# Performance work log

Hardware: AMD Instinct MI355X
Metric: run time of the kernel (lower is better)

The kernel has to match this reference:

```python
import jax, jax.numpy as jnp
import numpy as np

C1, C2, NUM_HEADS = 128, 128, 8
N, H_A, W_A = 2, 200, 200
H_B, W_B = 100, 360


def _polar_coords(fov, gh, gw, H, W):
    # Pixel-space polar sampling grid, matching torch linspace semantics.
    cx, cy = W // 2, H // 2
    t = jnp.arange(gw, dtype=jnp.float32) / (gw - 1)
    angles = -fov / 2 + fov * t                      # [gw]
    ca, sa = jnp.cos(angles), jnp.sin(angles)
    rmax = jnp.minimum(cx / jnp.abs(ca), cy / jnp.abs(sa))
    r = (jnp.arange(gh, dtype=jnp.float32) / (gh - 1))[:, None] * rmax[None, :]  # [gh,gw]
    x = jnp.clip(cx + r * ca, 0.0, W - 1.0)
    y = jnp.clip(cy - r * sa, 0.0, H - 1.0)
    return x, y


def _bilinear(bev, x, y):
    # grid_sample(mode='bilinear', align_corners=True) with in-range clamped coords.
    C, H, W = bev.shape
    x0 = jnp.floor(x); y0 = jnp.floor(y)
    wx = x - x0; wy = y - y0
    x0i = jnp.clip(x0.astype(jnp.int32), 0, W - 1)
    x1i = jnp.clip(x0i + 1, 0, W - 1)
    y0i = jnp.clip(y0.astype(jnp.int32), 0, H - 1)
    y1i = jnp.clip(y0i + 1, 0, H - 1)
    v00 = bev[:, y0i, x0i]; v01 = bev[:, y0i, x1i]
    v10 = bev[:, y1i, x0i]; v11 = bev[:, y1i, x1i]
    return v00 * (1 - wx) * (1 - wy) + v01 * wx * (1 - wy) + v10 * (1 - wx) * wy + v11 * wx * wy


def _restore(rect, fov, H, W):
    # scatter-add restore with count normalization (rrestore_bev_map).
    C, gh, gw = rect.shape
    x, y = _polar_coords(fov, gh, gw, H, W)
    xi = jnp.clip(jnp.round(x).astype(jnp.int32), 0, W - 1)
    yi = jnp.clip(jnp.round(y).astype(jnp.int32), 0, H - 1)
    idx = (yi * W + xi).reshape(-1)
    vals = rect.reshape(C, -1)
    acc = jnp.zeros((C, H * W), rect.dtype).at[:, idx].add(vals)
    cnt = jnp.zeros((H * W,), rect.dtype).at[idx].add(jnp.ones_like(idx, rect.dtype))
    cnt = jnp.where(cnt == 0, jnp.ones_like(cnt), cnt)
    return (acc / cnt).reshape(C, H, W)


def _mha(q, k, v, in_w, in_b, out_w, out_b, nheads):
    # torch.nn.MultiheadAttention (batch_first, eval mode -> dropout inactive).
    B, Lq, E = q.shape
    Lk = k.shape[1]
    hd = E // nheads
    wq, wk, wv = jnp.split(in_w, 3)
    bq, bk, bv = jnp.split(in_b, 3)
    qh = (q @ wq.T + bq).reshape(B, Lq, nheads, hd).transpose(0, 2, 1, 3)
    kh = (k @ wk.T + bk).reshape(B, Lk, nheads, hd).transpose(0, 2, 1, 3)
    vh = (v @ wv.T + bv).reshape(B, Lk, nheads, hd).transpose(0, 2, 1, 3)
    scores = jnp.einsum('bhqd,bhkd->bhqk', qh, kh) / jnp.sqrt(jnp.asarray(hd, q.dtype))
    attn = jax.nn.softmax(scores, axis=-1)
    o = jnp.einsum('bhqk,bhkd->bhqd', attn, vh).transpose(0, 2, 1, 3).reshape(B, Lq, E)
    return o @ out_w.T + out_b


def setup_inputs() -> dict:
    key = jax.random.key(0)
    ks = jax.random.split(key, 12)
    s1 = 1.0 / np.sqrt(C1)
    s2 = 1.0 / np.sqrt(C2)
    return {
        'list_a': jax.random.normal(ks[0], (N, C1, H_A, W_A), jnp.float32),
        'list_b': jax.random.normal(ks[1], (N, C2, H_B, W_B), jnp.float32),
        'fov_list': jax.random.uniform(ks[2], (N,), jnp.float32, 0.5 * np.pi, 0.9 * np.pi),
        'rots_list': jax.random.normal(ks[3], (N, 3, 3), jnp.float32),
        'trans_list': jax.random.normal(ks[4], (N, 3), jnp.float32),
        'Wq': jax.random.normal(ks[5], (C1, C1), jnp.float32) * s1,
        'bq': jnp.zeros((C1,), jnp.float32),
        'Wk': jax.random.normal(ks[6], (C1, C2), jnp.float32) * s2,
        'bk': jnp.zeros((C1,), jnp.float32),
        'Wv': jax.random.normal(ks[7], (C1, C2), jnp.float32) * s2,
        'bv': jnp.zeros((C1,), jnp.float32),
        'in_proj_w': jax.random.normal(ks[8], (3 * C1, C1), jnp.float32) * s1,
        'in_proj_b': jnp.zeros((3 * C1,), jnp.float32),
        'out_w': jax.random.normal(ks[9], (C1, C1), jnp.float32) * s1,
        'out_b': jnp.zeros((C1,), jnp.float32),
    }


def reference(list_a, list_b, fov_list, rots_list, trans_list,
              Wq, bq, Wk, bk, Wv, bv, in_proj_w, in_proj_b, out_w, out_b):
    def per_sample(a, b, fov):
        c1, h1, w1 = a.shape
        c2, h2, w2 = b.shape
        # extract rectangular (polar resample) of a onto (h1, w2) grid
        x, y = _polar_coords(fov, h1, w2, h1, w1)
        a_rect = _bilinear(a, x, y)                 # [C1, h1, w2]
        a_seq = a_rect.transpose(2, 1, 0)           # [w2, h1, C1]
        b_seq = b.transpose(2, 1, 0)                # [w2, h2, C2]
        q = a_seq @ Wq.T + bq
        k = b_seq @ Wk.T + bk
        v = b_seq @ Wv.T + bv
        o = _mha(q, k, v, in_proj_w, in_proj_b, out_w, out_b, NUM_HEADS)
        a_enh = o.transpose(2, 1, 0)                # [C1, h1, w2]
        return a + _restore(a_enh, fov, h1, w1)
    return jax.vmap(per_sample)(list_a, list_b, fov_list)
```

## Files before the change

### kernel.cpp

```cpp
#include <hip/hip_runtime.h>
#include <hip/hip_bf16.h>
#include <math.h>

#define C1N 128
#define HA 200
#define WA 200
#define HBB 100
#define WBB 360
#define GH 200
#define GW 360
#define NHD 8
#define HDD 16

typedef __attribute__((ext_vector_type(8))) short short8;
typedef __attribute__((ext_vector_type(4))) float f32x4;
typedef __attribute__((ext_vector_type(16))) float f32x16;

__device__ __forceinline__ float bf2f(unsigned short u) {
  union { unsigned int i; float f; } c; c.i = ((unsigned int)u) << 16; return c.f;
}
__device__ __forceinline__ unsigned short f2bf(float f) {
  __hip_bfloat16 h = __float2bfloat16(f);
  unsigned short u;
  __builtin_memcpy(&u, &h, sizeof(u));
  return u;
}

__device__ __forceinline__ void polar_xy(float fov, int i, int j, float& x, float& y) {
#pragma clang fp contract(off)
  float t = (float)j / 359.0f;
  float angle = -fov / 2.0f + fov * t;
  float ca = (float)cos((double)angle);
  float sa = (float)sin((double)angle);
  float rmax = fminf(100.0f / fabsf(ca), 100.0f / fabsf(sa));
  float r = ((float)i / 199.0f) * rmax;
  float xv = 100.0f + r * ca;
  float yv = 100.0f - r * sa;
  x = fminf(fmaxf(xv, 0.0f), 199.0f);
  y = fminf(fmaxf(yv, 0.0f), 199.0f);
}

__global__ void weff_k(const float* __restrict__ Wq, const float* __restrict__ Wk,
                       const float* __restrict__ Wv, const float* __restrict__ bq,
                       const float* __restrict__ bk, const float* __restrict__ bv,
                       const float* __restrict__ inw, const float* __restrict__ inb,
                       const float* __restrict__ outw, const float* __restrict__ outb,
                       __hip_bfloat16* __restrict__ Wb, float* __restrict__ beff) {
  int which = blockIdx.y;
  int o = blockIdx.x;
  int kcol = threadIdx.x;
  if (which == 3) {
    Wb[3 * 16384 + o * 128 + kcol] = __float2bfloat16(outw[o * 128 + kcol]);
    if (kcol == 0) beff[384 + o] = outb[o];
    return;
  }
  const float* Wx = (which == 0) ? Wq : ((which == 1) ? Wk : Wv);
  const float* bx = (which == 0) ? bq : ((which == 1) ? bk : bv);
  const float* wrow = inw + (which * 128 + o) * 128;
  float acc = 0.0f;
  for (int m = 0; m < 128; ++m) acc += wrow[m] * Wx[m * 128 + kcol];
  Wb[which * 16384 + o * 128 + kcol] = __float2bfloat16(acc);
  if (kcol == 0) {
    float bacc = inb[which * 128 + o];
    for (int m = 0; m < 128; ++m) bacc += wrow[m] * bx[m];
    beff[which * 128 + o] = bacc;
  }
}

__global__ __launch_bounds__(256) void transA_k(const float* __restrict__ a,
                                                __hip_bfloat16* __restrict__ aT) {
  __shared__ float tile[32][33];
  int p0 = blockIdx.x * 32, c0 = blockIdx.y * 32;
  int tp = threadIdx.x & 31, tr = threadIdx.x >> 5;
  for (int cc = tr; cc < 32; cc += 8)
    tile[cc][tp] = a[(size_t)(c0 + cc) * 40000 + p0 + tp];
  __syncthreads();
  for (int pp = tr; pp < 32; pp += 8)
    aT[(size_t)(p0 + pp) * C1N + c0 + tp] = __float2bfloat16(tile[tp][pp]);
}

__global__ __launch_bounds__(256) void bilinear2_k(const __hip_bfloat16* __restrict__ aT,
                                                   const float* __restrict__ fovp, int n,
                                                   __hip_bfloat16* __restrict__ aseq) {
  __shared__ float sw[20][4];
  __shared__ int sp[20][4];
  int j = blockIdx.x;
  int i_base = blockIdx.y * 20;
  int t = threadIdx.x;
  if (t < 20) {
    float x, y;
    polar_xy(fovp[n], i_base + t, j, x, y);
    float x0f = floorf(x), y0f = floorf(y);
    float wx = x - x0f, wy = y - y0f;
    int x0 = max(0, min(199, (int)x0f));
    int x1 = min(x0 + 1, 199);
    int y0 = max(0, min(199, (int)y0f));
    int y1 = min(y0 + 1, 199);
    sp[t][0] = y0 * 200 + x0; sp[t][1] = y0 * 200 + x1;
    sp[t][2] = y1 * 200 + x0; sp[t][3] = y1 * 200 + x1;
    sw[t][0] = (1.0f - wx) * (1.0f - wy); sw[t][1] = wx * (1.0f - wy);
    sw[t][2] = (1.0f - wx) * wy;          sw[t][3] = wx * wy;
  }
  __syncthreads();
  int lane = t & 63, wv = t >> 6;
  for (int ii = wv; ii < 20; ii += 4) {
    int i = i_base + ii;
    float w00 = sw[ii][0], w01 = sw[ii][1], w10 = sw[ii][2], w11 = sw[ii][3];
    ushort2 u00 = ((const ushort2*)(aT + (size_t)sp[ii][0] * C1N))[lane];
    ushort2 u01 = ((const ushort2*)(aT + (size_t)sp[ii][1] * C1N))[lane];
    ushort2 u10 = ((const ushort2*)(aT + (size_t)sp[ii][2] * C1N))[lane];
    ushort2 u11 = ((const ushort2*)(aT + (size_t)sp[ii][3] * C1N))[lane];
    float v0 = w00 * bf2f(u00.x) + w01 * bf2f(u01.x) + w10 * bf2f(u10.x) + w11 * bf2f(u11.x);
    float v1 = w00 * bf2f(u00.y) + w01 * bf2f(u01.y) + w10 * bf2f(u10.y) + w11 * bf2f(u11.y);
    ushort2 outv; outv.x = f2bf(v0); outv.y = f2bf(v1);
    ((ushort2*)(aseq + (size_t)(j * GH + i) * C1N))[lane] = outv;
  }
}

__global__ __launch_bounds__(256) void transpose_k(const float* __restrict__ b,
                                                   __hip_bfloat16* __restrict__ bs) {
  __shared__ float tile[32][33];
  int kk = blockIdx.z;
  int j0 = blockIdx.x * 32, c0 = blockIdx.y * 32;
  int tj = threadIdx.x & 31;
  int tr = threadIdx.x >> 5;
  for (int cc = tr; cc < 32; cc += 8) {
    int gj = j0 + tj;
    tile[cc][tj] = (gj < WBB) ? b[(c0 + cc) * (HBB * WBB) + kk * WBB + gj] : 0.0f;
  }
  __syncthreads();
  for (int jj = tr; jj < 32; jj += 8) {
    int gj = j0 + jj;
    if (gj < WBB)
      bs[(size_t)(gj * HBB + kk) * C1N + c0 + (threadIdx.x & 31)] =
          __float2bfloat16(tile[threadIdx.x & 31][jj]);
  }
}

__device__ __forceinline__ void gemm16_mfma(const unsigned short* __restrict__ A,
                                            const unsigned short* __restrict__ W,
                                            int m_base, f32x4 acc[8]) {
  int lane = threadIdx.x & 63;
  int col = lane & 15, quad = lane >> 4;
#pragma unroll
  for (int nt = 0; nt < 8; ++nt) acc[nt] = (f32x4)0.0f;
#pragma unroll
  for (int s = 0; s < 4; ++s) {
    short8 aF = *(const short8*)&A[(size_t)(m_base + col) * 128 + s * 32 + quad * 8];
#pragma unroll
    for (int nt = 0; nt < 8; ++nt) {
      short8 bF = *(const short8*)&W[(size_t)(nt * 16 + col) * 128 + s * 32 + quad * 8];
      acc[nt] = __builtin_amdgcn_mfma_f32_16x16x32_bf16(aF, bF, acc[nt], 0, 0, 0);
    }
  }
}

__device__ __forceinline__ void stage_bf16(unsigned short (*tile)[136],
                                           const f32x4 acc[8],
                                           const float* __restrict__ bias) {
  int lane = threadIdx.x & 63, wv = threadIdx.x >> 6;
  int col = lane & 15, quad = lane >> 4;
#pragma unroll
  for (int nt = 0; nt < 8; ++nt) {
    float bb = bias[nt * 16 + col];
#pragma unroll
    for (int r = 0; r < 4; ++r)
      tile[wv * 16 + quad * 4 + r][nt * 16 + col] = f2bf(acc[nt][r] + bb);
  }
  __syncthreads();
}

__global__ __launch_bounds__(256) void gemm_kv_k(const unsigned short* __restrict__ A,
                                                 const unsigned short* __restrict__ Wb,
                                                 const float* __restrict__ beff,
                                                 unsigned short* __restrict__ kb,
                                                 unsigned short* __restrict__ vT) {
  __shared__ unsigned short tile[64][136];
  int which = blockIdx.y;
  int m0 = blockIdx.x * 64;
  f32x4 acc[8];
  gemm16_mfma(A, Wb + (which ? 32768 : 16384), m0 + (threadIdx.x >> 6) * 16, acc);
  stage_bf16(tile, acc, beff + (which ? 256 : 128));
  if (which == 0) {
    for (int u = threadIdx.x; u < 1024; u += 256) {
      int rl = u >> 4, ch = (u & 15) * 8;
      int row = m0 + rl;
      if (row < 36000) {
        int jj = row / 100, key = row - jj * 100;
        *(short8*)&kb[((size_t)jj * 128 + key) * 128 + ch] = *(const short8*)&tile[rl][ch];
      }
    }
  } else {
    for (int u = threadIdx.x; u < 8192; u += 256) {
      int cc = u >> 6, kl = u & 63;
      int row = m0 + kl;
      if (row < 36000) {
        int jj = row / 100, key = row - jj * 100;
        vT[((size_t)jj * 128 + cc) * 128 + key] = tile[kl][cc];
      }
    }
  }
}

__global__ __launch_bounds__(512) void attn8_k(unsigned short* __restrict__ aseq_o,
                                               const unsigned short* __restrict__ kb,
                                               const unsigned short* __restrict__ vT,
                                               const unsigned short* __restrict__ Wb,
                                               const float* __restrict__ beff) {
  __shared__ unsigned short qos[32][136];
  int d = blockIdx.x;
  int xcd = d & 7, idx = d >> 3;
  int j = xcd * 45 + idx % 45;
  int mt = idx / 45;
  int h = threadIdx.x >> 6;
  int lane = threadIdx.x & 63;
  int col = lane & 31, half = lane >> 5;
  int col16 = lane & 15, quad = lane >> 4;

  {
    int rs = h & 1;
    int ng = h >> 1;
    int m_base = j * 200 + mt * 32 + rs * 16;
    f32x4 qacc[2];
    qacc[0] = (f32x4)0.0f; qacc[1] = (f32x4)0.0f;
#pragma unroll
    for (int s = 0; s < 4; ++s) {
      short8 aF = *(const short8*)&aseq_o[(size_t)(m_base + col16) * 128 + s * 32 + quad * 8];
#pragma unroll
      for (int i = 0; i < 2; ++i) {
        int nt = ng * 2 + i;
        short8 bF = *(const short8*)&Wb[(size_t)(nt * 16 + col16) * 128 + s * 32 + quad * 8];
        qacc[i] = __builtin_amdgcn_mfma_f32_16x16x32_bf16(aF, bF, qacc[i], 0, 0, 0);
      }
    }
#pragma unroll
    for (int i = 0; i < 2; ++i) {
      int nt = ng * 2 + i;
      float bb = beff[nt * 16 + col16];
#pragma unroll
      for (int r = 0; r < 4; ++r)
        qos[rs * 16 + quad * 4 + r][nt * 16 + col16] = f2bf(qacc[i][r] + bb);
    }
  }
  __syncthreads();

  short8 qF = *(const short8*)&qos[col][h * 16 + half * 8];
  f32x16 S[4];
#pragma unroll
  for (int nt = 0; nt < 4; ++nt) {
    short8 kF = *(const short8*)&kb[((size_t)j * 128 + nt * 32 + col) * 128 + h * 16 + half * 8];
    S[nt] = __builtin_amdgcn_mfma_f32_32x32x16_bf16(kF, qF, (f32x16)0.0f, 0, 0, 0);
  }

  float rsum = 0.0f;
#pragma unroll
  for (int nt = 0; nt < 3; ++nt)
#pragma unroll
    for (int r = 0; r < 16; ++r) {
      float e = __expf(S[nt][r] * 0.25f);
      S[nt][r] = e; rsum += e;
    }
#pragma unroll
  for (int r = 0; r < 16; ++r) {
    float e = (half == 0 && r < 4) ? __expf(S[3][r] * 0.25f) : 0.0f;
    S[3][r] = e; rsum += e;
  }
  rsum += __shfl_xor(rsum, 32, 64);
  float inv = __fdividef(1.0f, rsum);

  short8 ones;
#pragma unroll
  for (int i = 0; i < 8; ++i) ones[i] = (short)0x3F80;
  const unsigned short* vrow = &vT[((size_t)j * 128 + h * 16 + col16) * 128];
  f32x16 O = (f32x16)0.0f;
#pragma unroll
  for (int nt = 0; nt < 4; ++nt) {
    unsigned int ux[4], uy[4];
#pragma unroll
    for (int g = 0; g < 4; ++g) {
      if (nt == 3 && g >= 2) { ux[g] = 0; uy[g] = 0; continue; }
      float e0 = S[nt][4 * g + 0] * inv, e1 = S[nt][4 * g + 1] * inv;
      float e2 = S[nt][4 * g + 2] * inv, e3 = S[nt][4 * g + 3] * inv;
      asm("v_cvt_pk_bf16_f32 %0, %1, %2" : "=v"(ux[g]) : "v"(e0), "v"(e1));
      asm("v_cvt_pk_bf16_f32 %0, %1, %2" : "=v"(uy[g]) : "v"(e2), "v"(e3));
    }
#pragma unroll
    for (int p = 0; p < 2; ++p) {
      int ks = 2 * nt + p;
      if (ks >= 7) continue;
      unsigned int ax = ux[2 * p], bx = ux[2 * p + 1];
      asm("v_permlane32_swap_b32 %0, %1" : "+v"(ax), "+v"(bx));
      unsigned int ay = uy[2 * p], by = uy[2 * p + 1];
      asm("v_permlane32_swap_b32 %0, %1" : "+v"(ay), "+v"(by));
      union { unsigned int u4[4]; short8 s8; } cvt;
      cvt.u4[0] = ax; cvt.u4[1] = ay; cvt.u4[2] = bx; cvt.u4[3] = by;
      short8 bV = (col < 16) ? *(const short8*)&vrow[ks * 16 + half * 8] : ones;
      O = __builtin_amdgcn_mfma_f32_32x32x16_bf16(cvt.s8, bV, O, 0, 0, 0);
    }
  }

  __syncthreads();
#pragma unroll
  for (int r = 0; r < 16; ++r) {
    int row = (r & 3) + 8 * (r >> 2) + 4 * half;
    if (col < 16) qos[row][h * 16 + col] = f2bf(O[r]);
  }
  __syncthreads();
  int rl = threadIdx.x >> 4, ch = (threadIdx.x & 15) * 8;
  int qr = mt * 32 + rl;
  if (qr < 200)
    *(short8*)&aseq_o[(size_t)(j * 200 + qr) * 128 + ch] = *(const short8*)&qos[rl][ch];
}

__global__ __launch_bounds__(256) void zero_k(float* __restrict__ accP,
                                              float* __restrict__ cnt) {
  int t = blockIdx.x * 256 + threadIdx.x;
  for (int u = t; u < 1280000; u += 524288) ((f32x4*)accP)[u] = (f32x4)0.0f;
  if (t < 10000) ((f32x4*)cnt)[t] = (f32x4)0.0f;
}

__global__ __launch_bounds__(256) void gemm_os_k(const unsigned short* __restrict__ A,
                                                 const unsigned short* __restrict__ Wb,
                                                 const float* __restrict__ beff,
                                                 const float* __restrict__ fovp, int n,
                                                 float* __restrict__ accP,
                                                 float* __restrict__ cnt) {
  __shared__ float tile[64][132];
  __shared__ int sidx[64];
  int m0 = blockIdx.x * 64;
  int t = threadIdx.x;
  f32x4 acc[8];
  gemm16_mfma(A, Wb + 49152, m0 + (t >> 6) * 16, acc);
  if (t < 64) {
    int m = m0 + t;
    int j = m / 200, i = m - j * 200;
    float x, y;
    polar_xy(fovp[n], i, j, x, y);
    int xi = (int)rintf(x); xi = max(0, min(199, xi));
    int yi = (int)rintf(y); yi = max(0, min(199, yi));
    sidx[t] = yi * 200 + xi;
    atomicAdd(&cnt[yi * 200 + xi], 1.0f);
  }
  {
    int lane = t & 63, wv = t >> 6;
    int col = lane & 15, quad = lane >> 4;
#pragma unroll
    for (int nt = 0; nt < 8; ++nt) {
      float bb = beff[384 + nt * 16 + col];
#pragma unroll
      for (int r = 0; r < 4; ++r)
        tile[wv * 16 + quad * 4 + r][nt * 16 + col] = acc[nt][r] + bb;
    }
  }
  __syncthreads();
  int c = t & 127, half = t >> 7;
  int r0 = half * 32;
  int cur = sidx[r0];
  float sum = 0.0f;
#pragma unroll 4
  for (int r = r0; r < r0 + 32; ++r) {
    float v = tile[r][c];
    int idx = sidx[r];
    if (idx != cur) {
      atomicAdd(&accP[(size_t)cur * C1N + c], sum);
      cur = idx;
      sum = v;
    } else {
      sum += v;
    }
  }
  atomicAdd(&accP[(size_t)cur * C1N + c], sum);
}

__global__ __launch_bounds__(256) void finalize2_k(const float* __restrict__ a,
                                                   const float* __restrict__ accP,
                                                   const float* __restrict__ cnt,
                                                   float* __restrict__ out) {
  __shared__ float tile[64][129];
  __shared__ float sinv[64];
  int p0 = blockIdx.x * 64;
  int t = threadIdx.x;
  if (t < 64) {
    float cv = cnt[p0 + t];
    sinv[t] = 1.0f / (cv == 0.0f ? 1.0f : cv);
  }
  for (int u = t; u < 64 * 128; u += 256) {
    int pp = u >> 7, c = u & 127;
    tile[pp][c] = accP[(size_t)(p0 + pp) * C1N + c];
  }
  __syncthreads();
  for (int u = t; u < 64 * 128; u += 256) {
    int pp = u & 63, c = u >> 6;
    int g = c * 40000 + p0 + pp;
    out[g] = a[g] + tile[pp][c] * sinv[pp];
  }
}

extern "C" void kernel_launch(void* const* d_in, const int* in_sizes, int n_in,
                              void* d_out, int out_size, void* d_ws, size_t ws_size,
                              hipStream_t stream) {
  const float* list_a = (const float*)d_in[0];
  const float* list_b = (const float*)d_in[1];
  const float* fov   = (const float*)d_in[2];
  const float* Wq    = (const float*)d_in[5];
  const float* bq    = (const float*)d_in[6];
  const float* Wk    = (const float*)d_in[7];
  const float* bk    = (const float*)d_in[8];
  const float* Wv    = (const float*)d_in[9];
  const float* bv    = (const float*)d_in[10];
  const float* inw   = (const float*)d_in[11];
  const float* inb   = (const float*)d_in[12];
  const float* outw  = (const float*)d_in[13];
  const float* outb  = (const float*)d_in[14];
  float* out = (float*)d_out;
  float* ws = (float*)d_ws;

  float* beff = ws;
  __hip_bfloat16* Wb = (__hip_bfloat16*)(ws + 512);
  float* P2 = ws + 512 + 32768;
  float* qb_f = P2 + 9216000;
  float* kb_f = qb_f + 4620288;
  float* vT_f = kb_f + 2949120;
  float* P0_f = vT_f + 2949120;
  float* P1_f = P0_f + 4620288;
  float* cnt  = P1_f + 2310144;

  unsigned short* kb = (unsigned short*)kb_f;
  unsigned short* vT = (unsigned short*)vT_f;
  __hip_bfloat16* P0 = (__hip_bfloat16*)P0_f;
  __hip_bfloat16* P1 = (__hip_bfloat16*)P1_f;
  __hip_bfloat16* aT = (__hip_bfloat16*)P2;
  float* accP = P2;

  weff_k<<<dim3(128, 4), 128, 0, stream>>>(Wq, Wk, Wv, bq, bk, bv, inw, inb, outw, outb, Wb, beff);

  for (int n = 0; n < 2; ++n) {
    const float* a_n = list_a + (size_t)n * C1N * HA * WA;
    const float* b_n = list_b + (size_t)n * C1N * HBB * WBB;
    float* out_n = out + (size_t)n * C1N * HA * WA;

    transA_k<<<dim3(1250, 4), 256, 0, stream>>>(a_n, aT);
    bilinear2_k<<<dim3(GW, 10), 256, 0, stream>>>(aT, fov, n, P0);
    zero_k<<<2048, 256, 0, stream>>>(accP, cnt);
    transpose_k<<<dim3(12, 4, 100), 256, 0, stream>>>(b_n, P1);
    gemm_kv_k<<<dim3(563, 2), 256, 0, stream>>>((const unsigned short*)P1,
                                                (const unsigned short*)Wb, beff, kb, vT);
    attn8_k<<<2520, 512, 0, stream>>>((unsigned short*)P0, kb, vT,
                                      (const unsigned short*)Wb, beff);
    gemm_os_k<<<1125, 256, 0, stream>>>((const unsigned short*)P0,
                                        (const unsigned short*)Wb, beff, fov, n,
                                        accP, cnt);
    finalize2_k<<<625, 256, 0, stream>>>(a_n, accP, cnt, out_n);
  }
}
```

Before: 494.5 us.

## Batch both samples into single kernel launches with reorganized workspace

Replaces the per-sample host loop with kernels that take the batch index from a grid dimension, so each stage runs once over both samples. This halves launch count and doubles grid sizes, giving better GPU fill and fewer tail effects. The workspace is re-laid out so buffers can alias across stages (zeroing of the accumulators moves after attention, reusing the K/V region). The attention kernel also zeroes V entries beyond key 100 in the last k-step, which makes the padded keys contribute nothing.

```diff
diff --git a/kernel.cpp b/kernel.cpp
--- a/kernel.cpp
+++ b/kernel.cpp
@@ -11,6 +11,13 @@
 #define GW 360
 #define NHD 8
 #define HDD 16
+
+#define P0S 9240576
+#define KVS 11796480
+#define P1S 4620288
+#define ATS 5120000
+#define ACCS 5120000
+#define CNTS 40000
 
 typedef __attribute__((ext_vector_type(8))) short short8;
 typedef __attribute__((ext_vector_type(4))) float f32x4;
@@ -70,20 +77,26 @@
 __global__ __launch_bounds__(256) void transA_k(const float* __restrict__ a,
                                                 __hip_bfloat16* __restrict__ aT) {
   __shared__ float tile[32][33];
+  int n = blockIdx.z;
+  const float* an = a + (size_t)n * 5120000;
+  __hip_bfloat16* aTn = aT + (size_t)n * ATS;
   int p0 = blockIdx.x * 32, c0 = blockIdx.y * 32;
   int tp = threadIdx.x & 31, tr = threadIdx.x >> 5;
   for (int cc = tr; cc < 32; cc += 8)
-    tile[cc][tp] = a[(size_t)(c0 + cc) * 40000 + p0 + tp];
+    tile[cc][tp] = an[(size_t)(c0 + cc) * 40000 + p0 + tp];
   __syncthreads();
   for (int pp = tr; pp < 32; pp += 8)
-    aT[(size_t)(p0 + pp) * C1N + c0 + tp] = __float2bfloat16(tile[tp][pp]);
+    aTn[(size_t)(p0 + pp) * C1N + c0 + tp] = __float2bfloat16(tile[tp][pp]);
 }
 
 __global__ __launch_bounds__(256) void bilinear2_k(const __hip_bfloat16* __restrict__ aT,
-                                                   const float* __restrict__ fovp, int n,
+                                                   const float* __restrict__ fovp,
                                                    __hip_bfloat16* __restrict__ aseq) {
   __shared__ float sw[20][4];
   __shared__ int sp[20][4];
+  int n = blockIdx.z;
+  const __hip_bfloat16* aTn = aT + (size_t)n * ATS;
+  __hip_bfloat16* aseqn = aseq + (size_t)n * P0S;
   int j = blockIdx.x;
   int i_base = blockIdx.y * 20;
   int t = threadIdx.x;
@@ -106,33 +119,37 @@
   for (int ii = wv; ii < 20; ii += 4) {
     int i = i_base + ii;
     float w00 = sw[ii][0], w01 = sw[ii][1], w10 = sw[ii][2], w11 = sw[ii][3];
-    ushort2 u00 = ((const ushort2*)(aT + (size_t)sp[ii][0] * C1N))[lane];
-    ushort2 u01 = ((const ushort2*)(aT + (size_t)sp[ii][1] * C1N))[lane];
-    ushort2 u10 = ((const ushort2*)(aT + (size_t)sp[ii][2] * C1N))[lane];
-    ushort2 u11 = ((const ushort2*)(aT + (size_t)sp[ii][3] * C1N))[lane];
+    ushort2 u00 = ((const ushort2*)(aTn + (size_t)sp[ii][0] * C1N))[lane];
+    ushort2 u01 = ((const ushort2*)(aTn + (size_t)sp[ii][1] * C1N))[lane];
+    ushort2 u10 = ((const ushort2*)(aTn + (size_t)sp[ii][2] * C1N))[lane];
+    ushort2 u11 = ((const ushort2*)(aTn + (size_t)sp[ii][3] * C1N))[lane];
     float v0 = w00 * bf2f(u00.x) + w01 * bf2f(u01.x) + w10 * bf2f(u10.x) + w11 * bf2f(u11.x);
     float v1 = w00 * bf2f(u00.y) + w01 * bf2f(u01.y) + w10 * bf2f(u10.y) + w11 * bf2f(u11.y);
     ushort2 outv; outv.x = f2bf(v0); outv.y = f2bf(v1);
-    ((ushort2*)(aseq + (size_t)(j * GH + i) * C1N))[lane] = outv;
+    ((ushort2*)(aseqn + (size_t)(j * GH + i) * C1N))[lane] = outv;
   }
 }
 
 __global__ __launch_bounds__(256) void transpose_k(const float* __restrict__ b,
                                                    __hip_bfloat16* __restrict__ bs) {
   __shared__ float tile[32][33];
+  int bx = blockIdx.x;
+  int n = bx / 12;
+  const float* bn = b + (size_t)n * 4608000;
+  __hip_bfloat16* bsn = bs + (size_t)n * P1S;
   int kk = blockIdx.z;
-  int j0 = blockIdx.x * 32, c0 = blockIdx.y * 32;
+  int j0 = (bx % 12) * 32, c0 = blockIdx.y * 32;
   int tj = threadIdx.x & 31;
   int tr = threadIdx.x >> 5;
   for (int cc = tr; cc < 32; cc += 8) {
     int gj = j0 + tj;
-    tile[cc][tj] = (gj < WBB) ? b[(c0 + cc) * (HBB * WBB) + kk * WBB + gj] : 0.0f;
+    tile[cc][tj] = (gj < WBB) ? bn[(c0 + cc) * (HBB * WBB) + kk * WBB + gj] : 0.0f;
   }
   __syncthreads();
   for (int jj = tr; jj < 32; jj += 8) {
     int gj = j0 + jj;
     if (gj < WBB)
-      bs[(size_t)(gj * HBB + kk) * C1N + c0 + (threadIdx.x & 31)] =
+      bsn[(size_t)(gj * HBB + kk) * C1N + c0 + (threadIdx.x & 31)] =
           __float2bfloat16(tile[threadIdx.x & 31][jj]);
   }
 }
@@ -170,13 +187,17 @@
   __syncthreads();
 }
 
-__global__ __launch_bounds__(256) void gemm_kv_k(const unsigned short* __restrict__ A,
+__global__ __launch_bounds__(256) void gemm_kv_k(const unsigned short* __restrict__ P1b,
                                                  const unsigned short* __restrict__ Wb,
                                                  const float* __restrict__ beff,
-                                                 unsigned short* __restrict__ kb,
-                                                 unsigned short* __restrict__ vT) {
+                                                 unsigned short* __restrict__ kbB,
+                                                 unsigned short* __restrict__ vTB) {
   __shared__ unsigned short tile[64][136];
   int which = blockIdx.y;
+  int n = blockIdx.z;
+  const unsigned short* A = P1b + (size_t)n * P1S;
+  unsigned short* kb = kbB + (size_t)n * KVS;
+  unsigned short* vT = vTB + (size_t)n * KVS;
   int m0 = blockIdx.x * 64;
   f32x4 acc[8];
   gemm16_mfma(A, Wb + (which ? 32768 : 16384), m0 + (threadIdx.x >> 6) * 16, acc);
@@ -202,12 +223,16 @@
   }
 }
 
-__global__ __launch_bounds__(512) void attn8_k(unsigned short* __restrict__ aseq_o,
-                                               const unsigned short* __restrict__ kb,
-                                               const unsigned short* __restrict__ vT,
+__global__ __launch_bounds__(512) void attn9_k(unsigned short* __restrict__ P0b,
+                                               const unsigned short* __restrict__ kbB,
+                                               const unsigned short* __restrict__ vTB,
                                                const unsigned short* __restrict__ Wb,
                                                const float* __restrict__ beff) {
   __shared__ unsigned short qos[32][136];
+  int nS = blockIdx.y;
+  unsigned short* aseq_o = P0b + (size_t)nS * P0S;
+  const unsigned short* kb = kbB + (size_t)nS * KVS;
+  const unsigned short* vT = vTB + (size_t)nS * KVS;
   int d = blockIdx.x;
   int xcd = d & 7, idx = d >> 3;
   int j = xcd * 45 + idx % 45;
@@ -294,7 +319,20 @@
       asm("v_permlane32_swap_b32 %0, %1" : "+v"(ay), "+v"(by));
       union { unsigned int u4[4]; short8 s8; } cvt;
       cvt.u4[0] = ax; cvt.u4[1] = ay; cvt.u4[2] = bx; cvt.u4[3] = by;
-      short8 bV = (col < 16) ? *(const short8*)&vrow[ks * 16 + half * 8] : ones;
+      short8 bV;
+      if (col < 16) {
+        bV = *(const short8*)&vrow[ks * 16 + half * 8];
+        if (ks == 6) {
+          if (half) {
+#pragma unroll
+            for (int e = 0; e < 8; ++e) bV[e] = 0;
+          } else {
+            bV[4] = 0; bV[5] = 0; bV[6] = 0; bV[7] = 0;
+          }
+        }
+      } else {
+        bV = ones;
+      }
       O = __builtin_amdgcn_mfma_f32_32x32x16_bf16(cvt.s8, bV, O, 0, 0, 0);
     }
   }
@@ -312,21 +350,23 @@
     *(short8*)&aseq_o[(size_t)(j * 200 + qr) * 128 + ch] = *(const short8*)&qos[rl][ch];
 }
 
-__global__ __launch_bounds__(256) void zero_k(float* __restrict__ accP,
-                                              float* __restrict__ cnt) {
+__global__ __launch_bounds__(256) void zero_k(float* __restrict__ p) {
   int t = blockIdx.x * 256 + threadIdx.x;
-  for (int u = t; u < 1280000; u += 524288) ((f32x4*)accP)[u] = (f32x4)0.0f;
-  if (t < 10000) ((f32x4*)cnt)[t] = (f32x4)0.0f;
-}
-
-__global__ __launch_bounds__(256) void gemm_os_k(const unsigned short* __restrict__ A,
+  for (int u = t; u < 2580000; u += 524288) ((f32x4*)p)[u] = (f32x4)0.0f;
+}
+
+__global__ __launch_bounds__(256) void gemm_os_k(const unsigned short* __restrict__ P0b,
                                                  const unsigned short* __restrict__ Wb,
                                                  const float* __restrict__ beff,
-                                                 const float* __restrict__ fovp, int n,
-                                                 float* __restrict__ accP,
-                                                 float* __restrict__ cnt) {
+                                                 const float* __restrict__ fovp,
+                                                 float* __restrict__ accPB,
+                                                 float* __restrict__ cntB) {
   __shared__ float tile[64][132];
   __shared__ int sidx[64];
+  int n = blockIdx.y;
+  const unsigned short* A = P0b + (size_t)n * P0S;
+  float* accP = accPB + (size_t)n * ACCS;
+  float* cnt = cntB + (size_t)n * CNTS;
   int m0 = blockIdx.x * 64;
   int t = threadIdx.x;
   f32x4 acc[8];
@@ -373,11 +413,16 @@
 }
 
 __global__ __launch_bounds__(256) void finalize2_k(const float* __restrict__ a,
-                                                   const float* __restrict__ accP,
-                                                   const float* __restrict__ cnt,
+                                                   const float* __restrict__ accPB,
+                                                   const float* __restrict__ cntB,
                                                    float* __restrict__ out) {
   __shared__ float tile[64][129];
   __shared__ float sinv[64];
+  int n = blockIdx.y;
+  const float* an = a + (size_t)n * 5120000;
+  const float* accP = accPB + (size_t)n * ACCS;
+  const float* cnt = cntB + (size_t)n * CNTS;
+  float* outn = out + (size_t)n * 5120000;
   int p0 = blockIdx.x * 64;
   int t = threadIdx.x;
   if (t < 64) {
@@ -392,7 +437,7 @@
   for (int u = t; u < 64 * 128; u += 256) {
     int pp = u & 63, c = u >> 6;
     int g = c * 40000 + p0 + pp;
-    out[g] = a[g] + tile[pp][c] * sinv[pp];
+    outn[g] = an[g] + tile[pp][c] * sinv[pp];
   }
 }
 
@@ -417,39 +462,28 @@
 
   float* beff = ws;
   __hip_bfloat16* Wb = (__hip_bfloat16*)(ws + 512);
-  float* P2 = ws + 512 + 32768;
-  float* qb_f = P2 + 9216000;
-  float* kb_f = qb_f + 4620288;
-  float* vT_f = kb_f + 2949120;
-  float* P0_f = vT_f + 2949120;
-  float* P1_f = P0_f + 4620288;
-  float* cnt  = P1_f + 2310144;
-
-  unsigned short* kb = (unsigned short*)kb_f;
-  unsigned short* vT = (unsigned short*)vT_f;
-  __hip_bfloat16* P0 = (__hip_bfloat16*)P0_f;
-  __hip_bfloat16* P1 = (__hip_bfloat16*)P1_f;
-  __hip_bfloat16* aT = (__hip_bfloat16*)P2;
-  float* accP = P2;
+  float* S1f = ws + 33280;
+  float* S2f = S1f + 9240576;
+  float* S3f = S2f + 11796480;
+
+  unsigned short* P0b = (unsigned short*)S1f;
+  unsigned short* kbB = (unsigned short*)S2f;
+  unsigned short* vTB = (unsigned short*)(S2f + 2949120);
+  float* accPB = S2f;
+  float* cntB  = S2f + 2 * ACCS;
+  __hip_bfloat16* aTb = (__hip_bfloat16*)S3f;
+  unsigned short* P1b = (unsigned short*)S3f;
 
   weff_k<<<dim3(128, 4), 128, 0, stream>>>(Wq, Wk, Wv, bq, bk, bv, inw, inb, outw, outb, Wb, beff);
 
-  for (int n = 0; n < 2; ++n) {
-    const float* a_n = list_a + (size_t)n * C1N * HA * WA;
-    const float* b_n = list_b + (size_t)n * C1N * HBB * WBB;
-    float* out_n = out + (size_t)n * C1N * HA * WA;
-
-    transA_k<<<dim3(1250, 4), 256, 0, stream>>>(a_n, aT);
-    bilinear2_k<<<dim3(GW, 10), 256, 0, stream>>>(aT, fov, n, P0);
-    zero_k<<<2048, 256, 0, stream>>>(accP, cnt);
-    transpose_k<<<dim3(12, 4, 100), 256, 0, stream>>>(b_n, P1);
-    gemm_kv_k<<<dim3(563, 2), 256, 0, stream>>>((const unsigned short*)P1,
-                                                (const unsigned short*)Wb, beff, kb, vT);
-    attn8_k<<<2520, 512, 0, stream>>>((unsigned short*)P0, kb, vT,
-                                      (const unsigned short*)Wb, beff);
-    gemm_os_k<<<1125, 256, 0, stream>>>((const unsigned short*)P0,
-                                        (const unsigned short*)Wb, beff, fov, n,
-                                        accP, cnt);
-    finalize2_k<<<625, 256, 0, stream>>>(a_n, accP, cnt, out_n);
-  }
-}
+  transA_k<<<dim3(1250, 4, 2), 256, 0, stream>>>(list_a, aTb);
+  bilinear2_k<<<dim3(GW, 10, 2), 256, 0, stream>>>(aTb, fov, (__hip_bfloat16*)P0b);
+  transpose_k<<<dim3(24, 4, 100), 256, 0, stream>>>(list_b, (__hip_bfloat16*)P1b);
+  gemm_kv_k<<<dim3(563, 2, 2), 256, 0, stream>>>(P1b, (const unsigned short*)Wb, beff, kbB, vTB);
+  attn9_k<<<dim3(2520, 2), 512, 0, stream>>>(P0b, kbB, vTB,
+                                             (const unsigned short*)Wb, beff);
+  zero_k<<<2048, 256, 0, stream>>>(S2f);
+  gemm_os_k<<<dim3(1125, 2), 256, 0, stream>>>(P0b, (const unsigned short*)Wb, beff,
+                                               fov, accPB, cntB);
+  finalize2_k<<<dim3(625, 2), 256, 0, stream>>>(list_a, accPB, cntB, out);
+}
```

After: 466.7 us. 5.6% less time.
